# Kernel optimization log

Hardware: AMD Instinct MI355X
Metric: run time of the kernel (lower is better)

The kernel has to match this reference:

```python
import jax, jax.numpy as jnp
import numpy as np

K = 16
D = 1024
B = 65536

# Row-major off-diagonal index order matching the torch double loop (i, j, i != j)
_ii, _jj = np.nonzero(~np.eye(K, dtype=bool))  # each (K*(K-1),), row-major
OFF_I = jnp.asarray(_ii)
OFF_J = jnp.asarray(_jj)
DIAG = jnp.arange(K)


def setup_inputs() -> dict:
    key = jax.random.key(0)
    k1, k2, k3, k4, k5 = jax.random.split(key, 5)
    scale_d = 1.0 / np.sqrt(D)
    return {
        "x": jax.random.normal(k1, (B, D), dtype=jnp.float32),
        "Wd": jax.random.normal(k2, (K, D), dtype=jnp.float32) * scale_d,
        "bd": jax.random.normal(k3, (K,), dtype=jnp.float32) * 0.1,
        "Wo": jax.random.normal(k4, (K * (K - 1), D), dtype=jnp.float32) * scale_d,
        "bo": jax.random.normal(k5, (K * (K - 1),), dtype=jnp.float32) * 0.1 - 3.0,
    }


def reference(x, Wd, bd, Wo, bo):
    # Diagonal gates: (B, K)
    c_diag = jax.nn.sigmoid(jnp.einsum("bd,kd->bk", x, Wd) + bd)
    # Off-diagonal values: (B, K*(K-1)), non-positive
    off_vals = -jax.nn.softplus(jnp.einsum("bd,kd->bk", x, Wo) + bo)
    C = jnp.zeros((x.shape[0], K, K), dtype=x.dtype)
    C = C.at[:, OFF_I, OFF_J].set(off_vals)
    C = C.at[:, DIAG, DIAG].set(c_diag)
    return C
```

## Files before the change

kernel.cpp:

```cpp
#include <hip/hip_runtime.h>
#include <hip/hip_bf16.h>
#include <stdint.h>


typedef __bf16 bf16x8 __attribute__((ext_vector_type(8)));
typedef float f32x4 __attribute__((ext_vector_type(4)));

#define THREADS 512
#define BM 128
#define KSTEPS 32
#define WIMG 16384
#define WBYTES (WIMG * KSTEPS)

#define ASLOT 16384
#define BBASE 49152
#define BSLOT 16384
#define SMEM_SZ 81920

__device__ __forceinline__ unsigned bf_rtne(unsigned u) {
  return (u + 0x7fffu + ((u >> 16) & 1u)) >> 16;
}
__device__ __forceinline__ unsigned pack2(float lo, float hi) {
  return bf_rtne(__float_as_uint(lo)) | (bf_rtne(__float_as_uint(hi)) << 16);
}
__device__ __forceinline__ bf16x8 packfrag(const f32x4& a, const f32x4& b) {
  bf16x8 r;
  r[0] = (__bf16)a[0]; r[1] = (__bf16)a[1]; r[2] = (__bf16)a[2]; r[3] = (__bf16)a[3];
  r[4] = (__bf16)b[0]; r[5] = (__bf16)b[1]; r[6] = (__bf16)b[2]; r[7] = (__bf16)b[3];
  return r;
}
__device__ __forceinline__ void gload_lds16(const void* g, void* l) {
  __builtin_amdgcn_global_load_lds(
      (const __attribute__((address_space(1))) unsigned int*)g,
      (__attribute__((address_space(3))) unsigned int*)l, 16, 0, 0);
}

__global__ void prep_kernel(const float* __restrict__ Wd, const float* __restrict__ bd,
                            const float* __restrict__ Wo, const float* __restrict__ bo,
                            char* __restrict__ wbuf, float* __restrict__ bias) {
  const int c = blockIdx.x;
  const int t = threadIdx.x;
  const int i = c >> 4, j = c & 15;
  const float* src;
  float b;
  if (i == j) { src = Wd + i * 1024; b = bd[i]; }
  else { int r = i * 15 + (j < i ? j : j - 1); src = Wo + r * 1024; b = bo[r]; }
  if (t == 0) bias[c] = b;
  const int kk = t * 4;
  const int img = kk >> 5, k5 = kk & 31;
  float4 v = *reinterpret_cast<const float4*>(src + kk);
  uint2 h;
  h.x = pack2(v.x, v.y);
  h.y = pack2(v.z, v.w);
  const unsigned off = (unsigned)((c * 64 + k5 * 2) ^ (((c >> 1) & 3) << 4));
  *reinterpret_cast<uint2*>(wbuf + img * WIMG + off) = h;
}

__global__ __launch_bounds__(THREADS, 4) void cap_main(
    const float* __restrict__ x, const char* __restrict__ wbuf,
    const float* __restrict__ bias, float* __restrict__ out) {
  __shared__ char smem[SMEM_SZ];

  const int tid = threadIdx.x;
  const int wid = tid >> 6;
  const int lane = tid & 63;
  const int l15 = lane & 15;
  const int l4 = lane >> 4;
  const int wm = wid >> 2;
  const int wn = wid & 3;

  const size_t blkRow = (size_t)blockIdx.x * BM;

  const unsigned acol = (unsigned)(((tid & 7) * 16) ^ (((tid >> 3) & 7) << 4));
  const char* asrc[2];
  unsigned adst[2];
#pragma unroll
  for (int i = 0; i < 2; ++i) {
    const int row = i * 64 + (tid >> 3);
    asrc[i] = (const char*)(x + (blkRow + (size_t)row) * 1024) + acol;
    adst[i] = (unsigned)(i * 8192 + tid * 16);
  }

  const unsigned swA = (unsigned)((l15 & 7) << 4);
  const unsigned bbase = (unsigned)(wn * 4096 + l15 * 64 +
                                    ((l4 * 16) ^ (((l15 >> 1) & 3) << 4)));

  f32x4 acc[4][4];
#pragma unroll
  for (int m = 0; m < 4; ++m)
#pragma unroll
    for (int n = 0; n < 4; ++n) acc[m][n] = (f32x4){0.f, 0.f, 0.f, 0.f};

#define STAGE_A(CH, SL)                                                        \
  {                                                                            \
    _Pragma("unroll") for (int i = 0; i < 2; ++i)                              \
        gload_lds16(asrc[i] + (CH) * 128, smem + (SL) + adst[i]);              \
  }
#define STAGE_B(CH, SL)                                                        \
  {                                                                            \
    const char* wsp = wbuf + (CH) * WIMG;                                      \
    _Pragma("unroll") for (int i = 0; i < 2; ++i)                              \
        gload_lds16(wsp + i * 8192 + tid * 16,                                 \
                    smem + BBASE + (SL) + i * 8192 + tid * 16);                \
  }

  STAGE_A(0, 0);
  STAGE_B(0, 0);
  STAGE_A(1, ASLOT);
  asm volatile("s_waitcnt vmcnt(2)\n\ts_barrier" ::: "memory");

  unsigned aR = 0;
  unsigned aI = 2 * ASLOT;
  unsigned bR = 0;

  for (int t = 0; t < KSTEPS; ++t) {
    const int tb = (t + 1 < KSTEPS) ? t + 1 : KSTEPS - 1;
    STAGE_B(tb, bR ^ BSLOT);
    const int ta = (t + 2 < KSTEPS) ? t + 2 : KSTEPS - 1;
    STAGE_A(ta, aI);

    const char* Ac = smem + aR;
    const char* Bc = smem + BBASE + bR;
    bf16x8 af[4], bfr[4];
#pragma unroll
    for (int m = 0; m < 4; ++m) {
      const unsigned rb = (unsigned)((wm * 64 + m * 16 + l15) * 128);
      f32x4 u0 = *reinterpret_cast<const f32x4*>(Ac + rb + ((l4 * 32) ^ swA));
      f32x4 u1 = *reinterpret_cast<const f32x4*>(Ac + rb + ((l4 * 32 + 16) ^ swA));
      af[m] = packfrag(u0, u1);
    }
#pragma unroll
    for (int n = 0; n < 4; ++n)
      bfr[n] = *reinterpret_cast<const bf16x8*>(Bc + bbase + n * 1024);

#pragma unroll
    for (int m = 0; m < 4; ++m)
#pragma unroll
      for (int n = 0; n < 4; ++n)
        acc[m][n] = __builtin_amdgcn_mfma_f32_16x16x32_bf16(bfr[n], af[m], acc[m][n], 0, 0, 0);

    asm volatile("s_waitcnt vmcnt(2)" ::: "memory");
    asm volatile("s_waitcnt lgkmcnt(0)" ::: "memory");
    __builtin_amdgcn_s_barrier();

    aR = (aR == 2 * ASLOT) ? 0u : aR + ASLOT;
    aI = (aI == 2 * ASLOT) ? 0u : aI + ASLOT;
    bR ^= BSLOT;
  }
#undef STAGE_A
#undef STAGE_B

#pragma unroll
  for (int n = 0; n < 4; ++n) {
    const int colb = wn * 64 + n * 16 + l4 * 4;
    const float4 bb = *reinterpret_cast<const float4*>(bias + colb);
    const bool d0 = ((colb + 0) % 17) == 0;
    const bool d1 = ((colb + 1) % 17) == 0;
    const bool d2 = ((colb + 2) % 17) == 0;
    const bool d3 = ((colb + 3) % 17) == 0;
#pragma unroll
    for (int m = 0; m < 4; ++m) {
      const size_t row = blkRow + (size_t)(wm * 64 + m * 16 + l15);
      float4 o;
#pragma unroll
      for (int j2 = 0; j2 < 4; ++j2) {
        float v = acc[m][n][j2] + (&bb.x)[j2];
        float e = __expf(-fabsf(v));
        float sig = (v >= 0.f) ? 1.f / (1.f + e) : e / (1.f + e);
        float sp = fmaxf(v, 0.f) + __logf(1.f + e);
        const bool diag = j2 == 0 ? d0 : j2 == 1 ? d1 : j2 == 2 ? d2 : d3;
        (&o.x)[j2] = diag ? sig : -sp;
      }
      *reinterpret_cast<float4*>(out + row * 256 + colb) = o;
    }
  }
}

extern "C" void kernel_launch(void* const* d_in, const int* in_sizes, int n_in,
                              void* d_out, int out_size, void* d_ws, size_t ws_size,
                              hipStream_t stream) {
  const float* x = (const float*)d_in[0];
  const float* Wd = (const float*)d_in[1];
  const float* bd = (const float*)d_in[2];
  const float* Wo = (const float*)d_in[3];
  const float* bo = (const float*)d_in[4];
  float* out = (float*)d_out;
  char* wbuf = (char*)d_ws;
  float* bias = (float*)(wbuf + WBYTES);

  prep_kernel<<<dim3(256), dim3(256), 0, stream>>>(Wd, bd, Wo, bo, wbuf, bias);
  cap_main<<<dim3(512), dim3(THREADS), 0, stream>>>(x, wbuf, bias, out);
}
```

Baseline: 98.67 us.

## Read weights directly from global memory and stage A in 64-wide double buffers

Weight fragments now come straight from global memory (L2-resident) in a new fragment-friendly layout, so B no longer goes through LDS. The A tile is staged in two 32KB units each covering two k-steps, which halves the number of stage issues and cuts LDS to 64KB. The risk is added global-load latency on the weight path inside the inner loop, and the change from a three-slot to a two-slot A pipeline means less prefetch depth.

```diff
diff --git a/kernel.cpp b/kernel.cpp
--- a/kernel.cpp
+++ b/kernel.cpp
@@ -9,13 +9,10 @@
 #define THREADS 512
 #define BM 128
 #define KSTEPS 32
-#define WIMG 16384
-#define WBYTES (WIMG * KSTEPS)
+#define WBYTES 524288
 
-#define ASLOT 16384
-#define BBASE 49152
-#define BSLOT 16384
-#define SMEM_SZ 81920
+#define AUNIT 32768
+#define SMEM_SZ 65536
 
 __device__ __forceinline__ unsigned bf_rtne(unsigned u) {
   return (u + 0x7fffu + ((u >> 16) & 1u)) >> 16;
@@ -47,13 +44,12 @@
   else { int r = i * 15 + (j < i ? j : j - 1); src = Wo + r * 1024; b = bo[r]; }
   if (t == 0) bias[c] = b;
   const int kk = t * 4;
-  const int img = kk >> 5, k5 = kk & 31;
+  const int ch = kk >> 5, q = (kk >> 3) & 3, e = kk & 7;
   float4 v = *reinterpret_cast<const float4*>(src + kk);
   uint2 h;
   h.x = pack2(v.x, v.y);
   h.y = pack2(v.z, v.w);
-  const unsigned off = (unsigned)((c * 64 + k5 * 2) ^ (((c >> 1) & 3) << 4));
-  *reinterpret_cast<uint2*>(wbuf + img * WIMG + off) = h;
+  *reinterpret_cast<uint2*>(wbuf + ch * 16384 + q * 4096 + c * 16 + e * 2) = h;
 }
 
 __global__ __launch_bounds__(THREADS, 4) void cap_main(
@@ -71,19 +67,18 @@
 
   const size_t blkRow = (size_t)blockIdx.x * BM;
 
-  const unsigned acol = (unsigned)(((tid & 7) * 16) ^ (((tid >> 3) & 7) << 4));
-  const char* asrc[2];
-  unsigned adst[2];
+  const unsigned acol = (unsigned)(((tid & 15) * 16) ^ (((tid >> 4) & 15) << 4));
+  const char* asrc[4];
+  unsigned adst[4];
 #pragma unroll
-  for (int i = 0; i < 2; ++i) {
-    const int row = i * 64 + (tid >> 3);
+  for (int i = 0; i < 4; ++i) {
+    const int row = i * 32 + (tid >> 4);
     asrc[i] = (const char*)(x + (blkRow + (size_t)row) * 1024) + acol;
     adst[i] = (unsigned)(i * 8192 + tid * 16);
   }
 
-  const unsigned swA = (unsigned)((l15 & 7) << 4);
-  const unsigned bbase = (unsigned)(wn * 4096 + l15 * 64 +
-                                    ((l4 * 16) ^ (((l15 >> 1) & 3) << 4)));
+  const unsigned swA = (unsigned)(l15 << 4);
+  const char* wb = wbuf + l4 * 4096 + (wn * 64 + l15) * 16;
 
   f32x4 acc[4][4];
 #pragma unroll
@@ -91,64 +86,52 @@
 #pragma unroll
     for (int n = 0; n < 4; ++n) acc[m][n] = (f32x4){0.f, 0.f, 0.f, 0.f};
 
-#define STAGE_A(CH, SL)                                                        \
+#define STAGE_A2(SU, SL)                                                       \
   {                                                                            \
-    _Pragma("unroll") for (int i = 0; i < 2; ++i)                              \
-        gload_lds16(asrc[i] + (CH) * 128, smem + (SL) + adst[i]);              \
-  }
-#define STAGE_B(CH, SL)                                                        \
-  {                                                                            \
-    const char* wsp = wbuf + (CH) * WIMG;                                      \
-    _Pragma("unroll") for (int i = 0; i < 2; ++i)                              \
-        gload_lds16(wsp + i * 8192 + tid * 16,                                 \
-                    smem + BBASE + (SL) + i * 8192 + tid * 16);                \
+    _Pragma("unroll") for (int i = 0; i < 4; ++i)                              \
+        gload_lds16(asrc[i] + (SU) * 256, smem + (SL) + adst[i]);              \
   }
 
-  STAGE_A(0, 0);
-  STAGE_B(0, 0);
-  STAGE_A(1, ASLOT);
-  asm volatile("s_waitcnt vmcnt(2)\n\ts_barrier" ::: "memory");
+#define SUBSTEP(T, UNIT, P, VM)                                                \
+  {                                                                            \
+                                             \
+    const char* wt = wb + (T) * 16384;                                         \
+    bf16x8 bfr[4];                                                             \
+    _Pragma("unroll") for (int n = 0; n < 4; ++n)                              \
+        bfr[n] = *reinterpret_cast<const bf16x8*>(wt + n * 256);               \
+                                          \
+    const char* Ac = smem + (UNIT) * AUNIT;                                    \
+    bf16x8 af[4];                                                              \
+    _Pragma("unroll") for (int m = 0; m < 4; ++m) {                            \
+      const unsigned rb = (unsigned)((wm * 64 + m * 16 + l15) * 256);          \
+      f32x4 u0 = *reinterpret_cast<const f32x4*>(                              \
+          Ac + rb + (((P) * 128 + l4 * 32) ^ swA));                            \
+      f32x4 u1 = *reinterpret_cast<const f32x4*>(                              \
+          Ac + rb + (((P) * 128 + l4 * 32 + 16) ^ swA));                       \
+      af[m] = packfrag(u0, u1);                                                \
+    }                                                                          \
+    _Pragma("unroll") for (int m = 0; m < 4; ++m)                              \
+      _Pragma("unroll") for (int n = 0; n < 4; ++n)                            \
+        acc[m][n] = __builtin_amdgcn_mfma_f32_16x16x32_bf16(                   \
+            bfr[n], af[m], acc[m][n], 0, 0, 0);                                \
+    asm volatile("s_waitcnt vmcnt(" #VM ")" ::: "memory");                     \
+    asm volatile("s_waitcnt lgkmcnt(0)" ::: "memory");                         \
+    __builtin_amdgcn_s_barrier();                                              \
+  }
 
-  unsigned aR = 0;
-  unsigned aI = 2 * ASLOT;
-  unsigned bR = 0;
+  STAGE_A2(0, 0);
+  asm volatile("s_waitcnt vmcnt(0)" ::: "memory");
+  __builtin_amdgcn_s_barrier();
 
-  for (int t = 0; t < KSTEPS; ++t) {
-    const int tb = (t + 1 < KSTEPS) ? t + 1 : KSTEPS - 1;
-    STAGE_B(tb, bR ^ BSLOT);
-    const int ta = (t + 2 < KSTEPS) ? t + 2 : KSTEPS - 1;
-    STAGE_A(ta, aI);
-
-    const char* Ac = smem + aR;
-    const char* Bc = smem + BBASE + bR;
-    bf16x8 af[4], bfr[4];
-#pragma unroll
-    for (int m = 0; m < 4; ++m) {
-      const unsigned rb = (unsigned)((wm * 64 + m * 16 + l15) * 128);
-      f32x4 u0 = *reinterpret_cast<const f32x4*>(Ac + rb + ((l4 * 32) ^ swA));
-      f32x4 u1 = *reinterpret_cast<const f32x4*>(Ac + rb + ((l4 * 32 + 16) ^ swA));
-      af[m] = packfrag(u0, u1);
-    }
-#pragma unroll
-    for (int n = 0; n < 4; ++n)
-      bfr[n] = *reinterpret_cast<const bf16x8*>(Bc + bbase + n * 1024);
-
-#pragma unroll
-    for (int m = 0; m < 4; ++m)
-#pragma unroll
-      for (int n = 0; n < 4; ++n)
-        acc[m][n] = __builtin_amdgcn_mfma_f32_16x16x32_bf16(bfr[n], af[m], acc[m][n], 0, 0, 0);
-
-    asm volatile("s_waitcnt vmcnt(2)" ::: "memory");
-    asm volatile("s_waitcnt lgkmcnt(0)" ::: "memory");
-    __builtin_amdgcn_s_barrier();
-
-    aR = (aR == 2 * ASLOT) ? 0u : aR + ASLOT;
-    aI = (aI == 2 * ASLOT) ? 0u : aI + ASLOT;
-    bR ^= BSLOT;
+  for (int s = 0; s < KSTEPS / 2; ++s) {
+    const int su = (s + 1 < KSTEPS / 2) ? s + 1 : KSTEPS / 2 - 1;
+    const int cu = s & 1;
+    STAGE_A2(su, (cu ^ 1) * AUNIT);
+    SUBSTEP(2 * s, cu, 0, 4);
+    SUBSTEP(2 * s + 1, cu, 1, 0);
   }
-#undef STAGE_A
-#undef STAGE_B
+#undef STAGE_A2
+#undef SUBSTEP
 
 #pragma unroll
   for (int n = 0; n < 4; ++n) {
```

Measured after the change: 102.9 us. 1.04x slower.
